# Kernel tuning notes

Hardware: AMD Instinct MI355X
Metric: run time of the kernel (lower is better)

Reference implementation:

```python
import jax, jax.numpy as jnp
import numpy as np

B, T, C, H = 2, 2048, 1024, 16
D = C // H  # d_head = 64
SCALE = 1.0 / float(np.sqrt(D))


def setup_inputs() -> dict:
    key = jax.random.key(0)
    ks = jax.random.split(key, 9)
    s = 0.02  # small init so softmax isn't fully saturated
    inp = {
        "x": jax.random.normal(ks[0], (B, T, C), jnp.float32),
        # causal mask, broadcast over batch and heads; mask==0 positions are blocked
        "mask": jnp.tril(jnp.ones((T, T), jnp.int32))[None, None, :, :],
        "wq": jax.random.normal(ks[1], (C, C), jnp.float32) * s,
        "bq": jnp.zeros((C,), jnp.float32),
        "wk": jax.random.normal(ks[2], (C, C), jnp.float32) * s,
        "bk": jnp.zeros((C,), jnp.float32),
        "wv": jax.random.normal(ks[3], (C, C), jnp.float32) * s,
        "bv": jnp.zeros((C,), jnp.float32),
        "wo": jax.random.normal(ks[4], (C, C), jnp.float32) * s,
        "bo": jnp.zeros((C,), jnp.float32),
    }
    return inp


def reference(x, mask, wq, bq, wk, bk, wv, bv, wo, bo):
    Bx, Tx, Cx = x.shape
    # torch nn.Linear: y = x @ W.T + b
    def lin(z, w, b):
        return jnp.einsum("btc,oc->bto", z, w) + b

    def split_heads(z):  # [B,T,C] -> [B,H,T,D]
        return z.reshape(Bx, Tx, H, D).transpose(0, 2, 1, 3)

    q = split_heads(lin(x, wq, bq))
    k = split_heads(lin(x, wk, bk))
    v = split_heads(lin(x, wv, bv))

    scores = jnp.einsum("bhqd,bhkd->bhqk", q, k) * SCALE  # [B,H,T,T]
    scores = jnp.where(mask == 0, jnp.float32(-1e9), scores)
    probs = jax.nn.softmax(scores, axis=-1)

    # post-softmax entropy statistic (full T x T materialization, as in source)
    entropy = -(probs * jnp.log(probs + 1e-9)).sum(-1).mean()

    out = jnp.einsum("bhqk,bhkd->bhqd", probs, v)  # [B,H,T,D]
    out = out.transpose(0, 2, 1, 3).reshape(Bx, Tx, Cx)
    out = jnp.einsum("btc,oc->bto", out, wo) + bo
    return out, entropy
```

## Files before the change

### kernel.cpp

```cpp
#include <hip/hip_runtime.h>
#include <math.h>

typedef short bf8_t __attribute__((ext_vector_type(8)));
typedef float f4_t  __attribute__((ext_vector_type(4)));
typedef unsigned int u32;
typedef unsigned short u16;

#define MFMA(a,b,c) __builtin_amdgcn_mfma_f32_16x16x32_bf16((a),(b),(c),0,0,0)

__device__ __forceinline__ void gload16(const void* g, void* l) {
  __builtin_amdgcn_global_load_lds(
      (const __attribute__((address_space(1))) void*)g,
      (__attribute__((address_space(3))) void*)l, 16, 0, 0);
}

__device__ __forceinline__ u16 f2bf(float f) {
  u32 u = __float_as_uint(f);
  u += 0x7fff + ((u >> 16) & 1);
  return (u16)(u >> 16);
}

__device__ __forceinline__ u32 cvtpk(float a, float b) {
  u32 r;
  asm("v_cvt_pk_bf16_f32 %0, %1, %2" : "=v"(r) : "v"(a), "v"(b));
  return r;
}

__device__ __forceinline__ void gemm_tile(
    const u16* __restrict__ A, const u16* __restrict__ Bm,
    int lda, int ldb, int m0, int n0, int K,
    short* As, short* Bs, f4_t acc[4][4], int tid)
{
  const int lane = tid & 63, w = tid >> 6;
  const int lo = lane & 15, hi = lane >> 4;
  const int wr = (w >> 1) * 64, wc = (w & 1) * 64;
  for (int k0 = 0; k0 < K; k0 += 64) {
    __syncthreads();
#pragma unroll
    for (int iss = 0; iss < 4; ++iss) {
      int bb = iss * 4096 + tid * 16;
      int row = bb >> 7;
      int lg = ((bb >> 4) & 7) ^ (row & 7);
      gload16(A  + (size_t)(m0 + row) * lda + k0 + lg * 8,
              (char*)As + iss * 4096 + w * 1024);
      gload16(Bm + (size_t)(n0 + row) * ldb + k0 + lg * 8,
              (char*)Bs + iss * 4096 + w * 1024);
    }
    __syncthreads();
#pragma unroll
    for (int kk = 0; kk < 2; ++kk) {
      bf8_t af[4], bfr[4];
#pragma unroll
      for (int m = 0; m < 4; ++m) {
        int row = wr + m * 16 + lo;
        int g = (kk * 4 + hi) ^ (row & 7);
        af[m] = *(const bf8_t*)&As[row * 64 + g * 8];
      }
#pragma unroll
      for (int n = 0; n < 4; ++n) {
        int row = wc + n * 16 + lo;
        int g = (kk * 4 + hi) ^ (row & 7);
        bfr[n] = *(const bf8_t*)&Bs[row * 64 + g * 8];
      }
#pragma unroll
      for (int m = 0; m < 4; ++m)
#pragma unroll
        for (int n = 0; n < 4; ++n)
          acc[m][n] = MFMA(af[m], bfr[n], acc[m][n]);
    }
  }
}

__global__ __launch_bounds__(256)
void convert_kernel(const float* __restrict__ x,  const float* __restrict__ wq,
                    const float* __restrict__ wk, const float* __restrict__ wv,
                    const float* __restrict__ wo,
                    u16* xb, u16* wqb, u16* wkb, u16* wvb, u16* wob, float* ent)
{
  size_t i = (size_t)blockIdx.x * 256 + threadIdx.x;
  if (blockIdx.x == 0 && threadIdx.x == 0) *ent = 0.f;
  const float* src; u16* dst; size_t off;
  if (i < 524288) { src = x; dst = xb; off = i; }
  else {
    size_t r = i - 524288;
    int sel = (int)(r >> 17);
    off = r & 131071;
    src = sel == 0 ? wq : sel == 1 ? wk : sel == 2 ? wv : wo;
    dst = sel == 0 ? wqb : sel == 1 ? wkb : sel == 2 ? wvb : wob;
  }
  f4_t a = *(const f4_t*)&src[off * 8];
  f4_t c = *(const f4_t*)&src[off * 8 + 4];
  u16 t[8] = {f2bf(a[0]), f2bf(a[1]), f2bf(a[2]), f2bf(a[3]),
              f2bf(c[0]), f2bf(c[1]), f2bf(c[2]), f2bf(c[3])};
  *(uint4*)&dst[off * 8] = *(const uint4*)t;
}

__global__ __launch_bounds__(256)
void qkv_kernel(const u16* __restrict__ X, const u16* __restrict__ Wq,
                const u16* __restrict__ Wk, const u16* __restrict__ Wv,
                const float* __restrict__ bq, const float* __restrict__ bk,
                const float* __restrict__ bv,
                u16* Qo, u16* Ko, u16* Vto)
{
  __shared__ short smem[16384];
  short* As = smem;
  short* Bs = smem + 8192;
  const int tid = threadIdx.x;
  const int nb = blockIdx.x;
  const int which = nb >> 3;
  const int n0 = (nb & 7) * 128;
  const int m0 = blockIdx.y * 128;
  const u16* W    = which == 0 ? Wq : which == 1 ? Wk : Wv;
  const float* bias = which == 0 ? bq : which == 1 ? bk : bv;

  f4_t acc[4][4];
#pragma unroll
  for (int m = 0; m < 4; ++m)
#pragma unroll
    for (int n = 0; n < 4; ++n) acc[m][n] = f4_t{0.f, 0.f, 0.f, 0.f};

  gemm_tile(X, W, 1024, 1024, m0, n0, 1024, As, Bs, acc, tid);
  __syncthreads();

  const int lane = tid & 63, w = tid >> 6;
  const int lo = lane & 15, hi = lane >> 4;
  const int wr = (w >> 1) * 64, wc = (w & 1) * 64;
  const float scl = (which == 0) ? 0.125f : 1.0f;
  char* ep = (char*)smem;
  const int bix = m0 >> 11, t0g = m0 & 2047;

  if (which < 2) {
#pragma unroll
    for (int n = 0; n < 4; ++n) {
      int c = wc + n * 16 + lo;
      float bb = bias[n0 + c];
#pragma unroll
      for (int m = 0; m < 4; ++m)
#pragma unroll
        for (int j = 0; j < 4; ++j) {
          int r = wr + m * 16 + hi * 4 + j;
          int pg = (c >> 3) ^ ((r & 7) << 1);
          *(u16*)(ep + r * 256 + pg * 16 + (c & 7) * 2) =
              f2bf((acc[m][n][j] + bb) * scl);
        }
    }
    __syncthreads();
    u16* Out = (which == 0) ? Qo : Ko;
#pragma unroll
    for (int rep = 0; rep < 8; ++rep) {
      int r = rep * 16 + (tid >> 4);
      int seg = tid & 15;
      int pg = seg ^ ((r & 7) << 1);
      uint4 v = *(uint4*)(ep + r * 256 + pg * 16);
      int hh = (n0 >> 6) + (seg >> 3);
      int d = (seg & 7) * 8;
      *(uint4*)&Out[(((size_t)bix * 16 + hh) * 2048 + t0g + r) * 64 + d] = v;
    }
  } else {
#pragma unroll
    for (int n = 0; n < 4; ++n) {
      int c = wc + n * 16 + lo;
      float bb = bias[n0 + c];
#pragma unroll
      for (int m = 0; m < 4; ++m)
#pragma unroll
        for (int jp = 0; jp < 2; ++jp) {
          int r = wr + m * 16 + hi * 4 + jp * 2;
          u32 pk = cvtpk(acc[m][n][jp * 2] + bb, acc[m][n][jp * 2 + 1] + bb);
          int pg = (r >> 3) ^ ((c & 7) << 1);
          *(u32*)(ep + c * 256 + pg * 16 + (r & 7) * 2) = pk;
        }
    }
    __syncthreads();
#pragma unroll
    for (int rep = 0; rep < 8; ++rep) {
      int c = rep * 16 + (tid >> 4);
      int seg = tid & 15;
      int pg = seg ^ ((c & 7) << 1);
      uint4 v = *(uint4*)(ep + c * 256 + pg * 16);
      int f = n0 + c;
      int hh = f >> 6, d = f & 63;
      *(uint4*)&Vto[(((size_t)bix * 16 + hh) * 64 + d) * 2048 + t0g + seg * 8] = v;
    }
  }
}

__global__ __launch_bounds__(256, 4)
void attn_kernel(const u16* __restrict__ Qg, const u16* __restrict__ Kg,
                 const u16* __restrict__ Vtg, u16* __restrict__ Att,
                 float* __restrict__ Ent)
{
  __shared__ char smem[40960];
  const int tid = threadIdx.x, lane = tid & 63, w = tid >> 6;
  const int lo = lane & 15, hi = lane >> 4;
  const int n = blockIdx.x;
  const int bh = (n & 7) * 4 + ((n >> 3) & 3);
  const int g64 = 31 - (n >> 5);
  const int q0 = g64 * 64;
  const int nt = g64 + 1;
  const int b = bh >> 4, h = bh & 15;
  const u16* Qb  = Qg  + (size_t)bh * (2048 * 64);
  const u16* Kb  = Kg  + (size_t)bh * (2048 * 64);
  const u16* Vtb = Vtg + (size_t)bh * (64 * 2048);
  u16* Attp = Att + (size_t)b * (2048 * 1024) + h * 64;
  short* Pw = (short*)(smem + 32768 + w * 2048);

  const int qrow = q0 + w * 16 + lo;
  bf8_t qf[2];
#pragma unroll
  for (int kk = 0; kk < 2; ++kk)
    qf[kk] = *(const bf8_t*)&Qb[(size_t)qrow * 64 + kk * 32 + hi * 8];

  f4_t o[4];
#pragma unroll
  for (int md = 0; md < 4; ++md) o[md] = f4_t{0.f, 0.f, 0.f, 0.f};
  float m_ = -3.0e38f, l_ = 0.f, E_ = 0.f;

  auto STAGE = [&](int kt, int buf) {
#pragma unroll
    for (int iss = 0; iss < 2; ++iss) {
      int bb = iss * 4096 + tid * 16;
      int row = bb >> 7;
      int lg = ((bb >> 4) & 7) ^ (row & 7);
      gload16(Kb + (size_t)(kt * 64 + row) * 64 + lg * 8,
              smem + buf * 8192 + iss * 4096 + w * 1024);
      gload16(Vtb + (size_t)row * 2048 + kt * 64 + lg * 8,
              smem + 16384 + buf * 8192 + iss * 4096 + w * 1024);
    }
  };

  STAGE(0, 0);
  __syncthreads();
  int cur = 0;

  for (int kt = 0; kt < nt; ++kt) {
    if (kt + 1 < nt) STAGE(kt + 1, cur ^ 1);
    const short* KL = (const short*)(smem + cur * 8192);
    const short* VL = (const short*)(smem + 16384 + cur * 8192);

    f4_t s[4];
#pragma unroll
    for (int mk = 0; mk < 4; ++mk) s[mk] = f4_t{0.f, 0.f, 0.f, 0.f};
#pragma unroll
    for (int kk = 0; kk < 2; ++kk) {
      bf8_t kf[4];
#pragma unroll
      for (int mk = 0; mk < 4; ++mk) {
        int row = mk * 16 + lo;
        int gg = (kk * 4 + hi) ^ (row & 7);
        kf[mk] = *(const bf8_t*)&KL[row * 64 + gg * 8];
      }
#pragma unroll
      for (int mk = 0; mk < 4; ++mk)
        s[mk] = MFMA(kf[mk], qf[kk], s[mk]);
    }

    if (kt == nt - 1) {
#pragma unroll
      for (int mk = 0; mk < 4; ++mk)
#pragma unroll
        for (int jj = 0; jj < 4; ++jj)
          if ((mk * 16 + hi * 4 + jj) > (w * 16 + lo)) s[mk][jj] = -1.0e30f;
    }

    float mt = s[0][0];
#pragma unroll
    for (int mk = 0; mk < 4; ++mk)
#pragma unroll
      for (int jj = 0; jj < 4; ++jj) mt = fmaxf(mt, s[mk][jj]);
    mt = fmaxf(mt, __shfl_xor(mt, 16));
    mt = fmaxf(mt, __shfl_xor(mt, 32));
    if (!__all(mt <= m_ + 8.f)) {
      float mnew = fmaxf(m_, mt);
      float f = __expf(m_ - mnew);
      l_ *= f; E_ *= f;
#pragma unroll
      for (int md = 0; md < 4; ++md) o[md] *= f;
      m_ = mnew;
    }
    float p[16], lt = 0.f, Et = 0.f;
#pragma unroll
    for (int mk = 0; mk < 4; ++mk)
#pragma unroll
      for (int jj = 0; jj < 4; ++jj) {
        float pv = __expf(s[mk][jj] - m_);
        p[mk * 4 + jj] = pv;
        lt += pv; Et += pv * s[mk][jj];
      }
    lt += __shfl_xor(lt, 16); lt += __shfl_xor(lt, 32);
    Et += __shfl_xor(Et, 16); Et += __shfl_xor(Et, 32);
    l_ += lt; E_ += Et;

#pragma unroll
    for (int mk = 0; mk < 4; ++mk) {
      u32 a = cvtpk(p[mk * 4 + 0], p[mk * 4 + 1]);
      u32 c = cvtpk(p[mk * 4 + 2], p[mk * 4 + 3]);
      int gg = (mk * 2 + (hi >> 1)) ^ (lo & 7);
      *(uint2*)&Pw[lo * 64 + gg * 8 + (hi & 1) * 4] = make_uint2(a, c);
    }

#pragma unroll
    for (int kh = 0; kh < 2; ++kh) {
      int gp = (kh * 4 + hi) ^ (lo & 7);
      bf8_t pf = *(const bf8_t*)&Pw[lo * 64 + gp * 8];
#pragma unroll
      for (int md = 0; md < 4; ++md) {
        int row = md * 16 + lo;
        int gv = (kh * 4 + hi) ^ (row & 7);
        bf8_t vf = *(const bf8_t*)&VL[row * 64 + gv * 8];
        o[md] = MFMA(vf, pf, o[md]);
      }
    }
    __syncthreads();
    cur ^= 1;
  }

  float invl = 1.0f / l_;
#pragma unroll
  for (int md = 0; md < 4; ++md) {
    u32 w0 = cvtpk(o[md][0] * invl, o[md][1] * invl);
    u32 w1 = cvtpk(o[md][2] * invl, o[md][3] * invl);
    *(uint2*)&Attp[(size_t)qrow * 1024 + md * 16 + hi * 4] = make_uint2(w0, w1);
  }
  float hs = (hi == 0) ? (m_ + __logf(l_) - E_ * invl) : 0.f;
#pragma unroll
  for (int off = 1; off < 64; off <<= 1) hs += __shfl_xor(hs, off);
  if (lane == 0) atomicAdd(Ent, hs * (1.0f / 65536.0f));
}

__global__ __launch_bounds__(256)
void proj_kernel(const u16* __restrict__ Attb, const u16* __restrict__ Wo,
                 const float* __restrict__ bo, float* __restrict__ Out)
{
  __shared__ short smem[16384];
  short* As = smem;
  short* Bs = smem + 8192;
  const int tid = threadIdx.x;
  const int n0 = blockIdx.x * 128;
  const int m0 = blockIdx.y * 128;

  f4_t acc[4][4];
#pragma unroll
  for (int m = 0; m < 4; ++m)
#pragma unroll
    for (int n = 0; n < 4; ++n) acc[m][n] = f4_t{0.f, 0.f, 0.f, 0.f};

  gemm_tile(Attb, Wo, 1024, 1024, m0, n0, 1024, As, Bs, acc, tid);

  const int lane = tid & 63, w = tid >> 6;
  const int lo = lane & 15, hi = lane >> 4;
  const int wc = (w & 1) * 64;
  float* ep = (float*)smem;

#pragma unroll
  for (int pass = 0; pass < 2; ++pass) {
    __syncthreads();
    if ((w >> 1) == pass) {
#pragma unroll
      for (int n = 0; n < 4; ++n) {
        int c = wc + n * 16 + lo;
        float bb = bo[n0 + c];
#pragma unroll
        for (int m = 0; m < 4; ++m)
#pragma unroll
          for (int j = 0; j < 4; ++j) {
            int r = m * 16 + hi * 4 + j;
            int pg = (c >> 2) ^ ((r & 7) << 2);
            ep[r * 128 + pg * 4 + (c & 3)] = acc[m][n][j] + bb;
          }
      }
    }
    __syncthreads();
    int r = tid >> 2, q = tid & 3;
#pragma unroll
    for (int i = 0; i < 8; ++i) {
      int g = q * 8 + i;
      int pg = g ^ ((r & 7) << 2);
      f4_t v = *(f4_t*)&ep[r * 128 + pg * 4];
      *(f4_t*)&Out[(size_t)(m0 + pass * 64 + r) * 1024 + n0 + g * 4] = v;
    }
  }
}

extern "C" void kernel_launch(void* const* d_in, const int* in_sizes, int n_in,
                              void* d_out, int out_size, void* d_ws, size_t ws_size,
                              hipStream_t stream)
{
  const float* x  = (const float*)d_in[0];
  const float* wq = (const float*)d_in[2];
  const float* bq = (const float*)d_in[3];
  const float* wk = (const float*)d_in[4];
  const float* bk = (const float*)d_in[5];
  const float* wv = (const float*)d_in[6];
  const float* bv = (const float*)d_in[7];
  const float* wo = (const float*)d_in[8];
  const float* bo = (const float*)d_in[9];

  float* out = (float*)d_out;
  float* ent = out + (size_t)2 * 2048 * 1024;

  char* ws = (char*)d_ws;
  u16* xb   = (u16*)ws;
  u16* wqb  = (u16*)(ws + 8388608);
  u16* wkb  = (u16*)(ws + 8388608 + 2097152);
  u16* wvb  = (u16*)(ws + 8388608 + 2 * 2097152);
  u16* wob  = (u16*)(ws + 8388608 + 3 * 2097152);
  u16* Qb   = (u16*)(ws + 16777216);
  u16* Kb   = (u16*)(ws + 16777216 + 8388608);
  u16* Vtb  = (u16*)(ws + 16777216 + 2 * 8388608);
  u16* Attb = (u16*)(ws + 16777216 + 3 * 8388608);

  convert_kernel<<<4096, 256, 0, stream>>>(x, wq, wk, wv, wo,
                                           xb, wqb, wkb, wvb, wob, ent);
  qkv_kernel<<<dim3(24, 32), 256, 0, stream>>>(xb, wqb, wkb, wvb,
                                               bq, bk, bv, Qb, Kb, Vtb);
  attn_kernel<<<1024, 256, 0, stream>>>(Qb, Kb, Vtb, Attb, ent);
  proj_kernel<<<dim3(8, 32), 256, 0, stream>>>(Attb, wob, bo, out);
}
```

Measured before the change: 239.6 us.

## Double-buffer GEMM tiles and pair causal q-tiles per attention block

The shared GEMM tile loop now double-buffers A/B tiles in LDS, prefetching the next K step while computing the current one and dropping one barrier per step. This doubles shared memory use in the qkv and projection kernels. The attention kernel now processes two query tiles per block (tile p and tile 31-p), so every block does the same amount of causal work, and the grid is halved. Row-sum and entropy accumulators are reduced across lanes once at the end instead of every iteration. Occupancy may drop from the larger LDS footprint and from fewer attention blocks.

Result: faster. 223.0 us (-6.9%).

```diff
diff --git a/kernel.cpp b/kernel.cpp
--- a/kernel.cpp
+++ b/kernel.cpp
@@ -29,24 +29,34 @@
 __device__ __forceinline__ void gemm_tile(
     const u16* __restrict__ A, const u16* __restrict__ Bm,
     int lda, int ldb, int m0, int n0, int K,
-    short* As, short* Bs, f4_t acc[4][4], int tid)
+    short* smem, f4_t acc[4][4], int tid)
 {
   const int lane = tid & 63, w = tid >> 6;
   const int lo = lane & 15, hi = lane >> 4;
   const int wr = (w >> 1) * 64, wc = (w & 1) * 64;
-  for (int k0 = 0; k0 < K; k0 += 64) {
-    __syncthreads();
+  const int nsteps = K >> 6;
+
+  auto STAGE = [&](int step, int buf) {
+    int k0 = step * 64;
 #pragma unroll
     for (int iss = 0; iss < 4; ++iss) {
       int bb = iss * 4096 + tid * 16;
       int row = bb >> 7;
       int lg = ((bb >> 4) & 7) ^ (row & 7);
       gload16(A  + (size_t)(m0 + row) * lda + k0 + lg * 8,
-              (char*)As + iss * 4096 + w * 1024);
+              (char*)smem + buf * 16384 + iss * 4096 + w * 1024);
       gload16(Bm + (size_t)(n0 + row) * ldb + k0 + lg * 8,
-              (char*)Bs + iss * 4096 + w * 1024);
-    }
-    __syncthreads();
+              (char*)smem + 32768 + buf * 16384 + iss * 4096 + w * 1024);
+    }
+  };
+
+  STAGE(0, 0);
+  __syncthreads();
+  int cur = 0;
+  for (int step = 0; step < nsteps; ++step) {
+    if (step + 1 < nsteps) STAGE(step + 1, cur ^ 1);
+    const short* As = (const short*)((char*)smem + cur * 16384);
+    const short* Bs = (const short*)((char*)smem + 32768 + cur * 16384);
 #pragma unroll
     for (int kk = 0; kk < 2; ++kk) {
       bf8_t af[4], bfr[4];
@@ -68,6 +78,8 @@
         for (int n = 0; n < 4; ++n)
           acc[m][n] = MFMA(af[m], bfr[n], acc[m][n]);
     }
+    __syncthreads();
+    cur ^= 1;
   }
 }
 
@@ -102,9 +114,7 @@
                 const float* __restrict__ bv,
                 u16* Qo, u16* Ko, u16* Vto)
 {
-  __shared__ short smem[16384];
-  short* As = smem;
-  short* Bs = smem + 8192;
+  __shared__ short smem[32768];
   const int tid = threadIdx.x;
   const int nb = blockIdx.x;
   const int which = nb >> 3;
@@ -119,8 +129,7 @@
 #pragma unroll
     for (int n = 0; n < 4; ++n) acc[m][n] = f4_t{0.f, 0.f, 0.f, 0.f};
 
-  gemm_tile(X, W, 1024, 1024, m0, n0, 1024, As, Bs, acc, tid);
-  __syncthreads();
+  gemm_tile(X, W, 1024, 1024, m0, n0, 1024, smem, acc, tid);
 
   const int lane = tid & 63, w = tid >> 6;
   const int lo = lane & 15, hi = lane >> 4;
@@ -195,26 +204,13 @@
   const int lo = lane & 15, hi = lane >> 4;
   const int n = blockIdx.x;
   const int bh = (n & 7) * 4 + ((n >> 3) & 3);
-  const int g64 = 31 - (n >> 5);
-  const int q0 = g64 * 64;
-  const int nt = g64 + 1;
+  const int p = n >> 5;
   const int b = bh >> 4, h = bh & 15;
   const u16* Qb  = Qg  + (size_t)bh * (2048 * 64);
   const u16* Kb  = Kg  + (size_t)bh * (2048 * 64);
   const u16* Vtb = Vtg + (size_t)bh * (64 * 2048);
   u16* Attp = Att + (size_t)b * (2048 * 1024) + h * 64;
   short* Pw = (short*)(smem + 32768 + w * 2048);
-
-  const int qrow = q0 + w * 16 + lo;
-  bf8_t qf[2];
-#pragma unroll
-  for (int kk = 0; kk < 2; ++kk)
-    qf[kk] = *(const bf8_t*)&Qb[(size_t)qrow * 64 + kk * 32 + hi * 8];
-
-  f4_t o[4];
-#pragma unroll
-  for (int md = 0; md < 4; ++md) o[md] = f4_t{0.f, 0.f, 0.f, 0.f};
-  float m_ = -3.0e38f, l_ = 0.f, E_ = 0.f;
 
   auto STAGE = [&](int kt, int buf) {
 #pragma unroll
@@ -229,100 +225,122 @@
     }
   };
 
-  STAGE(0, 0);
-  __syncthreads();
-  int cur = 0;
-
-  for (int kt = 0; kt < nt; ++kt) {
-    if (kt + 1 < nt) STAGE(kt + 1, cur ^ 1);
-    const short* KL = (const short*)(smem + cur * 8192);
-    const short* VL = (const short*)(smem + 16384 + cur * 8192);
-
-    f4_t s[4];
-#pragma unroll
-    for (int mk = 0; mk < 4; ++mk) s[mk] = f4_t{0.f, 0.f, 0.f, 0.f};
-#pragma unroll
-    for (int kk = 0; kk < 2; ++kk) {
-      bf8_t kf[4];
+  float hs_total = 0.f;
+
+  for (int ph = 0; ph < 2; ++ph) {
+    const int g = ph ? (31 - p) : p;
+    const int q0 = g * 64;
+    const int nt = g + 1;
+    const int qrow = q0 + w * 16 + lo;
+
+    bf8_t qf[2];
+#pragma unroll
+    for (int kk = 0; kk < 2; ++kk)
+      qf[kk] = *(const bf8_t*)&Qb[(size_t)qrow * 64 + kk * 32 + hi * 8];
+
+    f4_t o[4];
+#pragma unroll
+    for (int md = 0; md < 4; ++md) o[md] = f4_t{0.f, 0.f, 0.f, 0.f};
+    float m_ = -3.0e38f, l_ = 0.f, E_ = 0.f;
+
+    STAGE(0, 0);
+    __syncthreads();
+    int cur = 0;
+
+    for (int kt = 0; kt < nt; ++kt) {
+      if (kt + 1 < nt) STAGE(kt + 1, cur ^ 1);
+      const short* KL = (const short*)(smem + cur * 8192);
+      const short* VL = (const short*)(smem + 16384 + cur * 8192);
+
+      f4_t s[4];
+#pragma unroll
+      for (int mk = 0; mk < 4; ++mk) s[mk] = f4_t{0.f, 0.f, 0.f, 0.f};
+#pragma unroll
+      for (int kk = 0; kk < 2; ++kk) {
+        bf8_t kf[4];
+#pragma unroll
+        for (int mk = 0; mk < 4; ++mk) {
+          int row = mk * 16 + lo;
+          int gg = (kk * 4 + hi) ^ (row & 7);
+          kf[mk] = *(const bf8_t*)&KL[row * 64 + gg * 8];
+        }
+#pragma unroll
+        for (int mk = 0; mk < 4; ++mk)
+          s[mk] = MFMA(kf[mk], qf[kk], s[mk]);
+      }
+
+      if (kt == nt - 1) {
+#pragma unroll
+        for (int mk = 0; mk < 4; ++mk)
+#pragma unroll
+          for (int jj = 0; jj < 4; ++jj)
+            if ((mk * 16 + hi * 4 + jj) > (w * 16 + lo)) s[mk][jj] = -1.0e30f;
+      }
+
+      float mt = s[0][0];
+#pragma unroll
+      for (int mk = 0; mk < 4; ++mk)
+#pragma unroll
+        for (int jj = 0; jj < 4; ++jj) mt = fmaxf(mt, s[mk][jj]);
+      mt = fmaxf(mt, __shfl_xor(mt, 16));
+      mt = fmaxf(mt, __shfl_xor(mt, 32));
+      if (!__all(mt <= m_ + 8.f)) {
+        float mnew = fmaxf(m_, mt);
+        float f = __expf(m_ - mnew);
+        l_ *= f; E_ *= f;
+#pragma unroll
+        for (int md = 0; md < 4; ++md) o[md] *= f;
+        m_ = mnew;
+      }
+      float pv16[16];
+#pragma unroll
+      for (int mk = 0; mk < 4; ++mk)
+#pragma unroll
+        for (int jj = 0; jj < 4; ++jj) {
+          float pv = __expf(s[mk][jj] - m_);
+          pv16[mk * 4 + jj] = pv;
+          l_ += pv; E_ += pv * s[mk][jj];
+        }
+
 #pragma unroll
       for (int mk = 0; mk < 4; ++mk) {
-        int row = mk * 16 + lo;
-        int gg = (kk * 4 + hi) ^ (row & 7);
-        kf[mk] = *(const bf8_t*)&KL[row * 64 + gg * 8];
-      }
-#pragma unroll
-      for (int mk = 0; mk < 4; ++mk)
-        s[mk] = MFMA(kf[mk], qf[kk], s[mk]);
-    }
-
-    if (kt == nt - 1) {
-#pragma unroll
-      for (int mk = 0; mk < 4; ++mk)
-#pragma unroll
-        for (int jj = 0; jj < 4; ++jj)
-          if ((mk * 16 + hi * 4 + jj) > (w * 16 + lo)) s[mk][jj] = -1.0e30f;
-    }
-
-    float mt = s[0][0];
-#pragma unroll
-    for (int mk = 0; mk < 4; ++mk)
-#pragma unroll
-      for (int jj = 0; jj < 4; ++jj) mt = fmaxf(mt, s[mk][jj]);
-    mt = fmaxf(mt, __shfl_xor(mt, 16));
-    mt = fmaxf(mt, __shfl_xor(mt, 32));
-    if (!__all(mt <= m_ + 8.f)) {
-      float mnew = fmaxf(m_, mt);
-      float f = __expf(m_ - mnew);
-      l_ *= f; E_ *= f;
-#pragma unroll
-      for (int md = 0; md < 4; ++md) o[md] *= f;
-      m_ = mnew;
-    }
-    float p[16], lt = 0.f, Et = 0.f;
-#pragma unroll
-    for (int mk = 0; mk < 4; ++mk)
-#pragma unroll
-      for (int jj = 0; jj < 4; ++jj) {
-        float pv = __expf(s[mk][jj] - m_);
-        p[mk * 4 + jj] = pv;
-        lt += pv; Et += pv * s[mk][jj];
-      }
-    lt += __shfl_xor(lt, 16); lt += __shfl_xor(lt, 32);
-    Et += __shfl_xor(Et, 16); Et += __shfl_xor(Et, 32);
-    l_ += lt; E_ += Et;
-
-#pragma unroll
-    for (int mk = 0; mk < 4; ++mk) {
-      u32 a = cvtpk(p[mk * 4 + 0], p[mk * 4 + 1]);
-      u32 c = cvtpk(p[mk * 4 + 2], p[mk * 4 + 3]);
-      int gg = (mk * 2 + (hi >> 1)) ^ (lo & 7);
-      *(uint2*)&Pw[lo * 64 + gg * 8 + (hi & 1) * 4] = make_uint2(a, c);
-    }
-
-#pragma unroll
-    for (int kh = 0; kh < 2; ++kh) {
-      int gp = (kh * 4 + hi) ^ (lo & 7);
-      bf8_t pf = *(const bf8_t*)&Pw[lo * 64 + gp * 8];
-#pragma unroll
-      for (int md = 0; md < 4; ++md) {
-        int row = md * 16 + lo;
-        int gv = (kh * 4 + hi) ^ (row & 7);
-        bf8_t vf = *(const bf8_t*)&VL[row * 64 + gv * 8];
-        o[md] = MFMA(vf, pf, o[md]);
-      }
-    }
-    __syncthreads();
-    cur ^= 1;
+        u32 a = cvtpk(pv16[mk * 4 + 0], pv16[mk * 4 + 1]);
+        u32 c = cvtpk(pv16[mk * 4 + 2], pv16[mk * 4 + 3]);
+        int gg = (mk * 2 + (hi >> 1)) ^ (lo & 7);
+        *(uint2*)&Pw[lo * 64 + gg * 8 + (hi & 1) * 4] = make_uint2(a, c);
+      }
+
+#pragma unroll
+      for (int kh = 0; kh < 2; ++kh) {
+        int gp = (kh * 4 + hi) ^ (lo & 7);
+        bf8_t pf = *(const bf8_t*)&Pw[lo * 64 + gp * 8];
+#pragma unroll
+        for (int md = 0; md < 4; ++md) {
+          int row = md * 16 + lo;
+          int gv = (kh * 4 + hi) ^ (row & 7);
+          bf8_t vf = *(const bf8_t*)&VL[row * 64 + gv * 8];
+          o[md] = MFMA(vf, pf, o[md]);
+        }
+      }
+      __syncthreads();
+      cur ^= 1;
+    }
+
+    l_ += __shfl_xor(l_, 16); l_ += __shfl_xor(l_, 32);
+    E_ += __shfl_xor(E_, 16); E_ += __shfl_xor(E_, 32);
+
+    float invl = 1.0f / l_;
+#pragma unroll
+    for (int md = 0; md < 4; ++md) {
+      u32 w0 = cvtpk(o[md][0] * invl, o[md][1] * invl);
+      u32 w1 = cvtpk(o[md][2] * invl, o[md][3] * invl);
+      *(uint2*)&Attp[(size_t)qrow * 1024 + md * 16 + hi * 4] =
+          make_uint2(w0, w1);
+    }
+    hs_total += (hi == 0) ? (m_ + __logf(l_) - E_ * invl) : 0.f;
   }
 
-  float invl = 1.0f / l_;
-#pragma unroll
-  for (int md = 0; md < 4; ++md) {
-    u32 w0 = cvtpk(o[md][0] * invl, o[md][1] * invl);
-    u32 w1 = cvtpk(o[md][2] * invl, o[md][3] * invl);
-    *(uint2*)&Attp[(size_t)qrow * 1024 + md * 16 + hi * 4] = make_uint2(w0, w1);
-  }
-  float hs = (hi == 0) ? (m_ + __logf(l_) - E_ * invl) : 0.f;
+  float hs = hs_total;
 #pragma unroll
   for (int off = 1; off < 64; off <<= 1) hs += __shfl_xor(hs, off);
   if (lane == 0) atomicAdd(Ent, hs * (1.0f / 65536.0f));
@@ -332,9 +350,7 @@
 void proj_kernel(const u16* __restrict__ Attb, const u16* __restrict__ Wo,
                  const float* __restrict__ bo, float* __restrict__ Out)
 {
-  __shared__ short smem[16384];
-  short* As = smem;
-  short* Bs = smem + 8192;
+  __shared__ short smem[32768];
   const int tid = threadIdx.x;
   const int n0 = blockIdx.x * 128;
   const int m0 = blockIdx.y * 128;
@@ -345,7 +361,7 @@
 #pragma unroll
     for (int n = 0; n < 4; ++n) acc[m][n] = f4_t{0.f, 0.f, 0.f, 0.f};
 
-  gemm_tile(Attb, Wo, 1024, 1024, m0, n0, 1024, As, Bs, acc, tid);
+  gemm_tile(Attb, Wo, 1024, 1024, m0, n0, 1024, smem, acc, tid);
 
   const int lane = tid & 63, w = tid >> 6;
   const int lo = lane & 15, hi = lane >> 4;
@@ -414,6 +430,6 @@
                                            xb, wqb, wkb, wvb, wob, ent);
   qkv_kernel<<<dim3(24, 32), 256, 0, stream>>>(xb, wqb, wkb, wvb,
                                                bq, bk, bv, Qb, Kb, Vtb);
-  attn_kernel<<<1024, 256, 0, stream>>>(Qb, Kb, Vtb, Attb, ent);
+  attn_kernel<<<512, 256, 0, stream>>>(Qb, Kb, Vtb, Attb, ent);
   proj_kernel<<<dim3(8, 32), 256, 0, stream>>>(Attb, wob, bo, out);
 }
```
